# Kernel optimization log

Measured on AMD Instinct MI355X. Metric: run time of the kernel, lower is better.

## Reference

```python
import jax, jax.numpy as jnp
import numpy as np

TEX_H = 256
TEX_W = 256
F_CH = 16
D_FACTOR = 0.5
DECAY = float(np.sqrt(2.0 * D_FACTOR * D_FACTOR))           # sqrt(d^2 + d^2)
AF = int(-np.log(0.1) * DECAY + 0.5)                        # active_field = 2
K = 2 * AF                                                  # 4x4 splat window


def setup_inputs() -> dict:
    key = jax.random.key(0)
    k1, k2, k3 = jax.random.split(key, 3)
    B, H, W = 8, 256, 256
    f_map = jax.random.normal(k1, (B, H, W, F_CH), dtype=jnp.float32)
    uv_map = jax.random.uniform(k2, (B, H, W, 2), dtype=jnp.float32)   # uv in [0,1)
    mask = (jax.random.uniform(k3, (B, H, W, 1)) < 0.5).astype(jnp.float32)
    return {"f_map": f_map, "uv_map": uv_map, "mask": mask}


def reference(f_map, uv_map, mask):
    B, H, W, C = f_map.shape
    N = B * H * W
    # uv_map[..., ::-1] * [tex_h, tex_w]: v comes from channel 1, u from channel 0
    v = (uv_map[..., 1] * TEX_H).reshape(N)
    u = (uv_map[..., 0] * TEX_W).reshape(N)
    pix = f_map.reshape(N, C)
    m = mask.reshape(N)  # 1 = masked pixel contributes (TF gathers where mask==1)

    v_shift = jnp.maximum(v - AF, 0.0)
    u_shift = jnp.maximum(u - AF, 0.0)
    offs = jnp.arange(K, dtype=jnp.float32)
    v_grid = v_shift[:, None, None] + offs[None, :, None]   # [N,K,K]
    u_grid = u_shift[:, None, None] + offs[None, None, :]   # [N,K,K]

    du = jnp.abs(u_grid - u[:, None, None])
    du = jnp.minimum(du, jnp.abs(du - TEX_W))               # wrap-around distance
    dv = jnp.abs(v_grid - v[:, None, None])
    dv = jnp.minimum(dv, jnp.abs(dv - TEX_H))
    wmap = jnp.exp(-jnp.sqrt(du * du + dv * dv) / DECAY)
    wmap = wmap * (wmap > 0.1) * m[:, None, None]           # threshold + mask gating

    vi = v_grid.astype(jnp.int32)
    ui = u_grid.astype(jnp.int32)
    valid = (vi < TEX_H) & (ui < TEX_W)                     # drop out-of-range splats
    wmap = wmap * valid
    idx = (jnp.clip(vi, 0, TEX_H - 1) * TEX_W + jnp.clip(ui, 0, TEX_W - 1)).reshape(-1)

    w_flat = wmap.reshape(-1)                               # [N*K*K]
    vals = (wmap.reshape(N, K * K)[..., None] * pix[:, None, :]).reshape(-1, C)

    wsum = jnp.zeros((TEX_H * TEX_W,), jnp.float32).at[idx].add(w_flat)
    csum = jnp.zeros((TEX_H * TEX_W, C), jnp.float32).at[idx].add(vals)
    wsum = wsum.reshape(TEX_H, TEX_W, 1)
    csum = csum.reshape(TEX_H, TEX_W, C)

    tex = (csum * (wsum > 0.01)) / (wsum + 0.001)           # weighted average
    return jnp.broadcast_to(tex[None], (B, TEX_H, TEX_W, C))
```

## Files before the change

### kernel.cpp

```cpp
#include <hip/hip_runtime.h>

#define TEX_H 256
#define TEX_W 256
#define FCH 16
#define NPIX (8 * 256 * 256)

#define SQRT2_F 1.41421356237f
#define W_EDGE   0.24311673443f
#define W_DIAG   0.13533528324f

#define HALO_C_OFF 0
#define HALO_N_OFF (256 * 256 * 16)
#define DIR_C_OFF  (HALO_N_OFF + 256 * 256)
#define DIR_W_OFF  (DIR_C_OFF + 2 * 4 * 256 * 16)
#define WS_FLOATS  (DIR_W_OFF + 2 * 4 * 256)

__global__ __launch_bounds__(256) void splat_kernel(
    const float*  __restrict__ f_map,
    const float2* __restrict__ uv_map,
    const float*  __restrict__ mask,
    float* __restrict__ ws)
{
    int tid = blockIdx.x * 256 + threadIdx.x;
    int pix = tid >> 4;
    int c   = tid & 15;

    if (mask[pix] == 0.0f) return;

    float2 uv = uv_map[pix];
    float u = uv.x * 256.0f;
    float v = uv.y * 256.0f;
    float f = f_map[pix * FCH + c];

    if (u >= 2.0f && v >= 2.0f) {
        int iu = (int)u, iv = (int)v;
        unsafeAtomicAdd(&ws[HALO_C_OFF + (iv * 256 + iu) * FCH + c], f);
        if (c == 0) unsafeAtomicAdd(&ws[HALO_N_OFF + iv * 256 + iu], 1.0f);
    } else {
        float us = fmaxf(u - 2.0f, 0.0f);
        float vs = fmaxf(v - 2.0f, 0.0f);
        #pragma unroll
        for (int kv = 0; kv < 4; ++kv) {
            float vg = vs + (float)kv;
            int vi = (int)vg;
            float dvf = fabsf(vg - v);
            #pragma unroll
            for (int ku = 0; ku < 4; ++ku) {
                float ug = us + (float)ku;
                int ui = (int)ug;
                float duf = fabsf(ug - u);
                float w = expf(-sqrtf(duf * duf + dvf * dvf) * SQRT2_F);
                if (w > 0.1f && vi < TEX_H && ui < TEX_W) {
                    int cell = (ui < 4) ? (ui * 256 + vi)
                                        : ((4 + vi) * 256 + ui);
                    unsafeAtomicAdd(&ws[DIR_C_OFF + cell * FCH + c], w * f);
                    if (c == 0) unsafeAtomicAdd(&ws[DIR_W_OFF + cell], w);
                }
            }
        }
    }
}

__global__ __launch_bounds__(256) void finalize_kernel(
    const float* __restrict__ ws,
    float* __restrict__ out)
{
    int tile = blockIdx.x;
    int r0 = (tile >> 5) << 3;
    int c0 = (tile & 31) << 3;
    int tx = threadIdx.x >> 2;
    int c4 = threadIdx.x & 3;
    int gr = r0 + (tx >> 3);
    int gc = c0 + (tx & 7);

    float4 cs = make_float4(0.f, 0.f, 0.f, 0.f);
    float wsm = 0.0f;

    #pragma unroll
    for (int a = -1; a <= 1; ++a) {
        int cr = gr + a;
        if (cr < 0 || cr > 255) continue;
        #pragma unroll
        for (int b = -1; b <= 1; ++b) {
            int cc = gc + b;
            if (cc < 0 || cc > 255) continue;
            float w = (a == 0 && b == 0) ? 1.0f
                    : ((a == 0 || b == 0) ? W_EDGE : W_DIAG);
            int cell = cr * 256 + cc;
            float4 h = *(const float4*)&ws[HALO_C_OFF + cell * FCH + c4 * 4];
            cs.x += w * h.x; cs.y += w * h.y; cs.z += w * h.z; cs.w += w * h.w;
            wsm  += w * ws[HALO_N_OFF + cell];
        }
    }

    if (gc < 4) {
        int cell = gc * 256 + gr;
        float4 d = *(const float4*)&ws[DIR_C_OFF + cell * FCH + c4 * 4];
        cs.x += d.x; cs.y += d.y; cs.z += d.z; cs.w += d.w;
        wsm  += ws[DIR_W_OFF + cell];
    } else if (gr < 4) {
        int cell = (4 + gr) * 256 + gc;
        float4 d = *(const float4*)&ws[DIR_C_OFF + cell * FCH + c4 * 4];
        cs.x += d.x; cs.y += d.y; cs.z += d.z; cs.w += d.w;
        wsm  += ws[DIR_W_OFF + cell];
    }

    float s = (wsm > 0.01f) ? (1.0f / (wsm + 0.001f)) : 0.0f;
    cs.x *= s; cs.y *= s; cs.z *= s; cs.w *= s;

    size_t base = ((size_t)gr * 256 + gc) * FCH + c4 * 4;
    #pragma unroll
    for (int b = 0; b < 8; ++b) {
        *(float4*)&out[(size_t)b * (256 * 256 * FCH) + base] = cs;
    }
}

extern "C" void kernel_launch(void* const* d_in, const int* in_sizes, int n_in,
                              void* d_out, int out_size, void* d_ws, size_t ws_size,
                              hipStream_t stream) {
    const float*  f_map  = (const float*)d_in[0];
    const float2* uv_map = (const float2*)d_in[1];
    const float*  mask   = (const float*)d_in[2];
    float* out = (float*)d_out;
    float* ws  = (float*)d_ws;

    hipMemsetAsync(ws, 0, (size_t)WS_FLOATS * sizeof(float), stream);

    splat_kernel<<<(NPIX * 16) / 256, 256, 0, stream>>>(f_map, uv_map, mask, ws);
    finalize_kernel<<<1024, 256, 0, stream>>>(ws, out);
}
```

Before: 61.29 us.

## Bin interior pixels into per-cell index buckets, then gather-sum without float atomics

Interior splats no longer do 16 float atomics per pixel straight into the cell accumulator. Each pixel now does one integer atomic to claim a slot in a per-cell bucket of capacity 16 and stores its index there. A new gather kernel then sums the feature vectors per cell and issues one atomic per channel. This aims to cut contended float atomic traffic, at the cost of an extra kernel launch, a larger workspace, a second read of f_map and a fallback path for overflowing buckets.

After: 65.02 us. +6.1%, slower.

```diff
diff --git a/kernel.cpp b/kernel.cpp
--- a/kernel.cpp
+++ b/kernel.cpp
@@ -4,16 +4,115 @@
 #define TEX_W 256
 #define FCH 16
 #define NPIX (8 * 256 * 256)
+#define NCELL (256 * 256)
+#define CAP 16
 
 #define SQRT2_F 1.41421356237f
 #define W_EDGE   0.24311673443f
 #define W_DIAG   0.13533528324f
 
 #define HALO_C_OFF 0
-#define HALO_N_OFF (256 * 256 * 16)
-#define DIR_C_OFF  (HALO_N_OFF + 256 * 256)
+#define HALO_N_OFF (NCELL * 16)
+#define DIR_C_OFF  (HALO_N_OFF + NCELL)
 #define DIR_W_OFF  (DIR_C_OFF + 2 * 4 * 256 * 16)
-#define WS_FLOATS  (DIR_W_OFF + 2 * 4 * 256)
+#define CNT_OFF    (DIR_W_OFF + 2 * 4 * 256)
+#define ENT_OFF    (CNT_OFF + NCELL)
+#define WS_FLOATS  (ENT_OFF + NCELL * CAP)
+#define ZERO_FLOATS ENT_OFF
+
+__device__ __forceinline__ void boundary_splat(float u, float v, float f, int c,
+                                               float* __restrict__ ws) {
+    float us = fmaxf(u - 2.0f, 0.0f);
+    float vs = fmaxf(v - 2.0f, 0.0f);
+    #pragma unroll
+    for (int kv = 0; kv < 4; ++kv) {
+        float vg = vs + (float)kv;
+        int vi = (int)vg;
+        float dvf = fabsf(vg - v);
+        #pragma unroll
+        for (int ku = 0; ku < 4; ++ku) {
+            float ug = us + (float)ku;
+            int ui = (int)ug;
+            float duf = fabsf(ug - u);
+            float w = expf(-sqrtf(duf * duf + dvf * dvf) * SQRT2_F);
+            if (w > 0.1f && vi < TEX_H && ui < TEX_W) {
+                int cell = (ui < 4) ? (ui * 256 + vi)
+                                    : ((4 + vi) * 256 + ui);
+                unsafeAtomicAdd(&ws[DIR_C_OFF + cell * FCH + c], w * f);
+                if (c == 0) unsafeAtomicAdd(&ws[DIR_W_OFF + cell], w);
+            }
+        }
+    }
+}
+
+__global__ __launch_bounds__(256) void bin_kernel(
+    const float*  __restrict__ f_map,
+    const float2* __restrict__ uv_map,
+    const float*  __restrict__ mask,
+    float* __restrict__ ws)
+{
+    int tid = blockIdx.x * 256 + threadIdx.x;
+    int pix = tid >> 4;
+    int c   = tid & 15;
+
+    if (mask[pix] == 0.0f) return;
+
+    float2 uv = uv_map[pix];
+    float u = uv.x * 256.0f;
+    float v = uv.y * 256.0f;
+
+    if (u >= 2.0f && v >= 2.0f) {
+        int cell = ((int)v) * 256 + (int)u;
+        int slot = 0;
+        if (c == 0) slot = atomicAdd((int*)ws + CNT_OFF + cell, 1);
+        slot = __shfl(slot, 0, 16);
+        if (slot < CAP) {
+            if (c == 0) ((unsigned*)ws)[ENT_OFF + cell * CAP + slot] = (unsigned)pix;
+        } else {
+            float f = f_map[pix * FCH + c];
+            unsafeAtomicAdd(&ws[HALO_C_OFF + cell * FCH + c], f);
+            if (c == 0) unsafeAtomicAdd(&ws[HALO_N_OFF + cell], 1.0f);
+        }
+    } else {
+        float f = f_map[pix * FCH + c];
+        boundary_splat(u, v, f, c, ws);
+    }
+}
+
+__global__ __launch_bounds__(256) void gather_kernel(
+    const float* __restrict__ f_map,
+    float* __restrict__ ws)
+{
+    int tid  = blockIdx.x * 256 + threadIdx.x;
+    int cell = tid >> 4;
+    int c    = tid & 15;
+
+    int cnt = min(((const int*)ws)[CNT_OFF + cell], CAP);
+    if (cnt == 0) return;
+
+    unsigned ent = ((const unsigned*)ws)[ENT_OFF + cell * CAP + c];
+    float acc = 0.0f;
+
+    int e = 0;
+    for (; e + 4 <= cnt; e += 4) {
+        unsigned p0 = __shfl(ent, e + 0, 16);
+        unsigned p1 = __shfl(ent, e + 1, 16);
+        unsigned p2 = __shfl(ent, e + 2, 16);
+        unsigned p3 = __shfl(ent, e + 3, 16);
+        float f0 = f_map[p0 * FCH + c];
+        float f1 = f_map[p1 * FCH + c];
+        float f2 = f_map[p2 * FCH + c];
+        float f3 = f_map[p3 * FCH + c];
+        acc += f0; acc += f1; acc += f2; acc += f3;
+    }
+    for (; e < cnt; ++e) {
+        unsigned p = __shfl(ent, e, 16);
+        acc += f_map[p * FCH + c];
+    }
+
+    unsafeAtomicAdd(&ws[HALO_C_OFF + cell * FCH + c], acc);
+    if (c == 0) unsafeAtomicAdd(&ws[HALO_N_OFF + cell], (float)cnt);
+}
 
 __global__ __launch_bounds__(256) void splat_kernel(
     const float*  __restrict__ f_map,
@@ -33,31 +132,11 @@
     float f = f_map[pix * FCH + c];
 
     if (u >= 2.0f && v >= 2.0f) {
-        int iu = (int)u, iv = (int)v;
-        unsafeAtomicAdd(&ws[HALO_C_OFF + (iv * 256 + iu) * FCH + c], f);
-        if (c == 0) unsafeAtomicAdd(&ws[HALO_N_OFF + iv * 256 + iu], 1.0f);
+        int cell = ((int)v) * 256 + (int)u;
+        unsafeAtomicAdd(&ws[HALO_C_OFF + cell * FCH + c], f);
+        if (c == 0) unsafeAtomicAdd(&ws[HALO_N_OFF + cell], 1.0f);
     } else {
-        float us = fmaxf(u - 2.0f, 0.0f);
-        float vs = fmaxf(v - 2.0f, 0.0f);
-        #pragma unroll
-        for (int kv = 0; kv < 4; ++kv) {
-            float vg = vs + (float)kv;
-            int vi = (int)vg;
-            float dvf = fabsf(vg - v);
-            #pragma unroll
-            for (int ku = 0; ku < 4; ++ku) {
-                float ug = us + (float)ku;
-                int ui = (int)ug;
-                float duf = fabsf(ug - u);
-                float w = expf(-sqrtf(duf * duf + dvf * dvf) * SQRT2_F);
-                if (w > 0.1f && vi < TEX_H && ui < TEX_W) {
-                    int cell = (ui < 4) ? (ui * 256 + vi)
-                                        : ((4 + vi) * 256 + ui);
-                    unsafeAtomicAdd(&ws[DIR_C_OFF + cell * FCH + c], w * f);
-                    if (c == 0) unsafeAtomicAdd(&ws[DIR_W_OFF + cell], w);
-                }
-            }
-        }
+        boundary_splat(u, v, f, c, ws);
     }
 }
 
@@ -124,8 +203,15 @@
     float* out = (float*)d_out;
     float* ws  = (float*)d_ws;
 
-    hipMemsetAsync(ws, 0, (size_t)WS_FLOATS * sizeof(float), stream);
-
-    splat_kernel<<<(NPIX * 16) / 256, 256, 0, stream>>>(f_map, uv_map, mask, ws);
+    bool bucketed = ws_size >= (size_t)WS_FLOATS * sizeof(float);
+
+    if (bucketed) {
+        hipMemsetAsync(ws, 0, (size_t)ZERO_FLOATS * sizeof(float), stream);
+        bin_kernel<<<(NPIX * 16) / 256, 256, 0, stream>>>(f_map, uv_map, mask, ws);
+        gather_kernel<<<(NCELL * 16) / 256, 256, 0, stream>>>(f_map, ws);
+    } else {
+        hipMemsetAsync(ws, 0, (size_t)CNT_OFF * sizeof(float), stream);
+        splat_kernel<<<(NPIX * 16) / 256, 256, 0, stream>>>(f_map, uv_map, mask, ws);
+    }
     finalize_kernel<<<1024, 256, 0, stream>>>(ws, out);
 }
```

## Accumulate halo features in packed half2 atomics and stage halo tiles in LDS

Applied to the files above, without the earlier changes.

The interior splat accumulator now holds fp16 pairs, so each thread issues one packed half2 atomic for two channels and launches half as many threads. The finalize kernel loads a 10x10 halo tile into shared memory once, instead of each thread reading the 3x3 neighbourhood from global memory, and writes the output with nontemporal stores. This is meant to cut atomic traffic, workspace size and memset cost, and redundant global reads. In exchange, accumulating in fp16 loses precision and can overflow at heavily hit cells, which risks accuracy against the fp32 reference.

New measurement: 60.79 us. Within noise of the previous version (-0.8%).

```diff
diff --git a/kernel.cpp b/kernel.cpp
--- a/kernel.cpp
+++ b/kernel.cpp
@@ -1,42 +1,54 @@
 #include <hip/hip_runtime.h>
+#include <hip/hip_fp16.h>
 
 #define TEX_H 256
 #define TEX_W 256
 #define FCH 16
 #define NPIX (8 * 256 * 256)
+#define NCELL (256 * 256)
 
 #define SQRT2_F 1.41421356237f
 #define W_EDGE   0.24311673443f
 #define W_DIAG   0.13533528324f
 
-#define HALO_C_OFF 0
-#define HALO_N_OFF (256 * 256 * 16)
-#define DIR_C_OFF  (HALO_N_OFF + 256 * 256)
-#define DIR_W_OFF  (DIR_C_OFF + 2 * 4 * 256 * 16)
-#define WS_FLOATS  (DIR_W_OFF + 2 * 4 * 256)
+typedef float vf4 __attribute__((ext_vector_type(4)));
+
+#define HALO_H_OFF 0
+#define HALO_N_OFF (NCELL * 16 * 2)
+#define DIR_C_OFF  (HALO_N_OFF + NCELL * 4)
+#define DIR_W_OFF  (DIR_C_OFF + 2048 * 16 * 4)
+#define ZERO_BYTES (DIR_W_OFF + 2048 * 4)
 
 __global__ __launch_bounds__(256) void splat_kernel(
     const float*  __restrict__ f_map,
     const float2* __restrict__ uv_map,
     const float*  __restrict__ mask,
-    float* __restrict__ ws)
+    char* __restrict__ wsb)
 {
+    __half2* halo = (__half2*)(wsb + HALO_H_OFF);
+    float*   hcnt = (float*)  (wsb + HALO_N_OFF);
+    float*   dirc = (float*)  (wsb + DIR_C_OFF);
+    float*   dirw = (float*)  (wsb + DIR_W_OFF);
+
     int tid = blockIdx.x * 256 + threadIdx.x;
-    int pix = tid >> 4;
-    int c   = tid & 15;
+    int pix = tid >> 3;
+    int l   = tid & 7;
 
     if (mask[pix] == 0.0f) return;
 
     float2 uv = uv_map[pix];
     float u = uv.x * 256.0f;
     float v = uv.y * 256.0f;
-    float f = f_map[pix * FCH + c];
 
     if (u >= 2.0f && v >= 2.0f) {
-        int iu = (int)u, iv = (int)v;
-        unsafeAtomicAdd(&ws[HALO_C_OFF + (iv * 256 + iu) * FCH + c], f);
-        if (c == 0) unsafeAtomicAdd(&ws[HALO_N_OFF + iv * 256 + iu], 1.0f);
+        int cell = ((int)v) * 256 + (int)u;
+        float2 fp = ((const float2*)f_map)[(size_t)pix * 8 + l];
+        __half2 h = __floats2half2_rn(fp.x, fp.y);
+        unsafeAtomicAdd(&halo[(size_t)cell * 8 + l], h);
+        if (l == 0) unsafeAtomicAdd(&hcnt[cell], 1.0f);
     } else {
+        float fa = f_map[(size_t)pix * FCH + l];
+        float fb = f_map[(size_t)pix * FCH + l + 8];
         float us = fmaxf(u - 2.0f, 0.0f);
         float vs = fmaxf(v - 2.0f, 0.0f);
         #pragma unroll
@@ -53,8 +65,9 @@
                 if (w > 0.1f && vi < TEX_H && ui < TEX_W) {
                     int cell = (ui < 4) ? (ui * 256 + vi)
                                         : ((4 + vi) * 256 + ui);
-                    unsafeAtomicAdd(&ws[DIR_C_OFF + cell * FCH + c], w * f);
-                    if (c == 0) unsafeAtomicAdd(&ws[DIR_W_OFF + cell], w);
+                    unsafeAtomicAdd(&dirc[(size_t)cell * FCH + l],     w * fa);
+                    unsafeAtomicAdd(&dirc[(size_t)cell * FCH + l + 8], w * fb);
+                    if (l == 0) unsafeAtomicAdd(&dirw[cell], w);
                 }
             }
         }
@@ -62,56 +75,75 @@
 }
 
 __global__ __launch_bounds__(256) void finalize_kernel(
-    const float* __restrict__ ws,
+    const char* __restrict__ wsb,
     float* __restrict__ out)
 {
+    const __half2* halo = (const __half2*)(wsb + HALO_H_OFF);
+    const float*   hcnt = (const float*)  (wsb + HALO_N_OFF);
+    const float*   dirc = (const float*)  (wsb + DIR_C_OFF);
+    const float*   dirw = (const float*)  (wsb + DIR_W_OFF);
+
+    __shared__ __half2 s_h[100][8];
+    __shared__ float   s_n[100];
+
     int tile = blockIdx.x;
     int r0 = (tile >> 5) << 3;
     int c0 = (tile & 31) << 3;
+
+    int i = threadIdx.x;
+    if (i < 200) {
+        int cellIdx = i >> 1, part = i & 1;
+        int hr = cellIdx / 10, hc = cellIdx - hr * 10;
+        int gr = r0 + hr - 1, gc = c0 + hc - 1;
+        uint4 val = make_uint4(0, 0, 0, 0);
+        bool inb = (gr >= 0) & (gr < 256) & (gc >= 0) & (gc < 256);
+        if (inb)
+            val = *(const uint4*)&halo[((size_t)gr * 256 + gc) * 8 + part * 4];
+        *(uint4*)&s_h[cellIdx][part * 4] = val;
+        if (part == 0) s_n[cellIdx] = inb ? hcnt[gr * 256 + gc] : 0.0f;
+    }
+    __syncthreads();
+
     int tx = threadIdx.x >> 2;
     int c4 = threadIdx.x & 3;
-    int gr = r0 + (tx >> 3);
-    int gc = c0 + (tx & 7);
+    int lr = tx >> 3, lc = tx & 7;
+    int gr = r0 + lr, gc = c0 + lc;
 
-    float4 cs = make_float4(0.f, 0.f, 0.f, 0.f);
+    vf4 cs = {0.f, 0.f, 0.f, 0.f};
     float wsm = 0.0f;
 
     #pragma unroll
-    for (int a = -1; a <= 1; ++a) {
-        int cr = gr + a;
-        if (cr < 0 || cr > 255) continue;
+    for (int a = 0; a < 3; ++a) {
         #pragma unroll
-        for (int b = -1; b <= 1; ++b) {
-            int cc = gc + b;
-            if (cc < 0 || cc > 255) continue;
-            float w = (a == 0 && b == 0) ? 1.0f
-                    : ((a == 0 || b == 0) ? W_EDGE : W_DIAG);
-            int cell = cr * 256 + cc;
-            float4 h = *(const float4*)&ws[HALO_C_OFF + cell * FCH + c4 * 4];
-            cs.x += w * h.x; cs.y += w * h.y; cs.z += w * h.z; cs.w += w * h.w;
-            wsm  += w * ws[HALO_N_OFF + cell];
+        for (int b = 0; b < 3; ++b) {
+            float w = (a == 1 && b == 1) ? 1.0f
+                    : ((a == 1 || b == 1) ? W_EDGE : W_DIAG);
+            int idx = (lr + a) * 10 + (lc + b);
+            float2 f0 = __half22float2(s_h[idx][c4 * 2 + 0]);
+            float2 f1 = __half22float2(s_h[idx][c4 * 2 + 1]);
+            cs.x += w * f0.x; cs.y += w * f0.y;
+            cs.z += w * f1.x; cs.w += w * f1.y;
+            wsm  += w * s_n[idx];
         }
     }
 
     if (gc < 4) {
         int cell = gc * 256 + gr;
-        float4 d = *(const float4*)&ws[DIR_C_OFF + cell * FCH + c4 * 4];
-        cs.x += d.x; cs.y += d.y; cs.z += d.z; cs.w += d.w;
-        wsm  += ws[DIR_W_OFF + cell];
+        cs += *(const vf4*)&dirc[(size_t)cell * FCH + c4 * 4];
+        wsm += dirw[cell];
     } else if (gr < 4) {
         int cell = (4 + gr) * 256 + gc;
-        float4 d = *(const float4*)&ws[DIR_C_OFF + cell * FCH + c4 * 4];
-        cs.x += d.x; cs.y += d.y; cs.z += d.z; cs.w += d.w;
-        wsm  += ws[DIR_W_OFF + cell];
+        cs += *(const vf4*)&dirc[(size_t)cell * FCH + c4 * 4];
+        wsm += dirw[cell];
     }
 
     float s = (wsm > 0.01f) ? (1.0f / (wsm + 0.001f)) : 0.0f;
-    cs.x *= s; cs.y *= s; cs.z *= s; cs.w *= s;
+    cs *= s;
 
     size_t base = ((size_t)gr * 256 + gc) * FCH + c4 * 4;
     #pragma unroll
     for (int b = 0; b < 8; ++b) {
-        *(float4*)&out[(size_t)b * (256 * 256 * FCH) + base] = cs;
+        __builtin_nontemporal_store(cs, (vf4*)&out[(size_t)b * (256 * 256 * FCH) + base]);
     }
 }
 
@@ -122,10 +154,10 @@
     const float2* uv_map = (const float2*)d_in[1];
     const float*  mask   = (const float*)d_in[2];
     float* out = (float*)d_out;
-    float* ws  = (float*)d_ws;
+    char*  wsb = (char*)d_ws;
 
-    hipMemsetAsync(ws, 0, (size_t)WS_FLOATS * sizeof(float), stream);
+    (void)hipMemsetAsync(wsb, 0, (size_t)ZERO_BYTES, stream);
 
-    splat_kernel<<<(NPIX * 16) / 256, 256, 0, stream>>>(f_map, uv_map, mask, ws);
-    finalize_kernel<<<1024, 256, 0, stream>>>(ws, out);
+    splat_kernel<<<(NPIX * 8) / 256, 256, 0, stream>>>(f_map, uv_map, mask, wsb);
+    finalize_kernel<<<1024, 256, 0, stream>>>(wsb, out);
 }
```
